# Optimization experiments

Hardware: AMD Instinct MI355X
Metric: run time of the kernel (lower is better)

## Reference

```python
import jax, jax.numpy as jnp
import numpy as np

ALPHA = 16.0
R = 8.0
SCALE = ALPHA / R  # scaling = alpha / r, same for every adapter


def setup_inputs() -> dict:
    key = jax.random.key(0)
    ks = jax.random.split(key, 5)
    B_, S, D = 4, 2048, 4096
    E, r = 8, 8
    x = jax.random.normal(ks[0], (B_, S, D), dtype=jnp.float32)
    W = jax.random.normal(ks[1], (D, D), dtype=jnp.float32) * (1.0 / np.sqrt(D))
    b = jax.random.normal(ks[2], (D,), dtype=jnp.float32) * 0.02
    A = jax.random.normal(ks[3], (E, r, D), dtype=jnp.float32) * (1.0 / np.sqrt(D))
    Bm = jax.random.normal(ks[4], (E, D, r), dtype=jnp.float32) * 0.02
    return {"x": x, "W": W, "b": b, "A": A, "B": Bm}


def reference(x, W, b, A, B):
    # base = F.linear(x, W, b)
    base = jnp.einsum('bsi,oi->bso', x, W) + b
    # lora_total = sum_e scale * (x @ A_e.T @ B_e.T); all experts stacked.
    # intermediate [B,S,E,r] is tiny (r=8)
    t = jnp.einsum('bsi,eri->bser', x, A)
    lora = jnp.einsum('bser,eor->bso', t, B) * SCALE
    return base + lora
```

## Files before the change

### kernel.cpp

```cpp
#include <hip/hip_runtime.h>
#include <hip/hip_bf16.h>

typedef unsigned short u16;
typedef __bf16 bf16x8 __attribute__((ext_vector_type(8)));
typedef float f32x4 __attribute__((ext_vector_type(4)));

constexpr int Mdim = 8192;
constexpr int Ndim = 4096;
constexpr int Kdim = 4096;
constexpr int ER   = 64;
constexpr float LSCALE = 2.0f;

__device__ __forceinline__ u16 f2bf(float f) {
    union { float f; unsigned u; } v; v.f = f;
    unsigned r = v.u + 0x7fffu + ((v.u >> 16) & 1u);
    return (u16)(r >> 16);
}

#define GLOAD_LDS16(g, l)                                             \
    __builtin_amdgcn_global_load_lds(                                 \
        (const __attribute__((address_space(1))) void*)(g),           \
        (__attribute__((address_space(3))) void*)(l), 16, 0, 0)

__global__ __launch_bounds__(256) void weff_kernel(
    const float* __restrict__ W, const float* __restrict__ A,
    const float* __restrict__ Bm, u16* __restrict__ Wb)
{
    __shared__ __align__(16) float sAc[ER][128];
    __shared__ __align__(16) float sBc[64][ER];

    const int t  = threadIdx.x;
    const int i0 = blockIdx.x * 128;
    const int o0 = blockIdx.y * 64;

#pragma unroll
    for (int p = 0; p < 8; ++p) {
        int lin = p * 1024 + t * 4;
        int er = lin >> 7, ci = lin & 127;
        *(float4*)&sAc[er][ci] = *(const float4*)(A + (size_t)er * Kdim + i0 + ci);
    }
    {
        int ol = t >> 2;
        int c  = (t & 3) * 16;
#pragma unroll
        for (int q = 0; q < 2; ++q) {
            int er = c + q * 8;
            int e  = er >> 3;
            const float* src = Bm + ((size_t)e * Ndim + (o0 + ol)) * 8;
            *(float4*)&sBc[ol][er]     = *(const float4*)(src);
            *(float4*)&sBc[ol][er + 4] = *(const float4*)(src + 4);
        }
    }
    __syncthreads();

    const int tx = t & 31;
    const int ty = t >> 5;
    float acc[8][4] = {};
#pragma unroll 4
    for (int er = 0; er < ER; ++er) {
        float4 a = *(const float4*)&sAc[er][tx * 4];
#pragma unroll
        for (int q = 0; q < 8; ++q) {
            float bv = sBc[q * 8 + ty][er];
            acc[q][0] += bv * a.x;
            acc[q][1] += bv * a.y;
            acc[q][2] += bv * a.z;
            acc[q][3] += bv * a.w;
        }
    }
#pragma unroll
    for (int q = 0; q < 8; ++q) {
        int o = o0 + q * 8 + ty;
        const float4 w = *(const float4*)(W + (size_t)o * Kdim + i0 + tx * 4);
        ushort4 st;
        st.x = f2bf(w.x + LSCALE * acc[q][0]);
        st.y = f2bf(w.y + LSCALE * acc[q][1]);
        st.z = f2bf(w.z + LSCALE * acc[q][2]);
        st.w = f2bf(w.w + LSCALE * acc[q][3]);
        *(ushort4*)(Wb + (size_t)o * Kdim + i0 + tx * 4) = st;
    }
}

__global__ __launch_bounds__(256) void cvt_x_kernel(
    const float* __restrict__ x, u16* __restrict__ xb)
{
    size_t i = (size_t)blockIdx.x * blockDim.x + threadIdx.x;
    const float4 v0 = *(const float4*)(x + i * 8);
    const float4 v1 = *(const float4*)(x + i * 8 + 4);
    uint4 o;
    o.x = (unsigned)f2bf(v0.x) | ((unsigned)f2bf(v0.y) << 16);
    o.y = (unsigned)f2bf(v0.z) | ((unsigned)f2bf(v0.w) << 16);
    o.z = (unsigned)f2bf(v1.x) | ((unsigned)f2bf(v1.y) << 16);
    o.w = (unsigned)f2bf(v1.z) | ((unsigned)f2bf(v1.w) << 16);
    *(uint4*)(xb + i * 8) = o;
}

constexpr int BM = 256, BN = 256, BK = 64;
constexpr int NT = Kdim / BK;

__global__ __launch_bounds__(512, 2) void gemm_bias_kernel(
    const u16* __restrict__ Xb, const u16* __restrict__ Wb,
    const float* __restrict__ bias, float* __restrict__ C)
{
    __shared__ __align__(16) u16 lds[65536];

    const int t    = threadIdx.x;
    const int lane = t & 63;
    const int wv   = t >> 6;
    const int wr   = wv >> 2;
    const int wc   = wv & 3;

    const int wg  = blockIdx.x;
    const int xcd = wg & 7, lid = wg >> 3;
    const int mt  = (xcd & 1) * 16 + (lid >> 2);
    const int ntl = (xcd >> 1) * 4 + (lid & 3);
    const int bm  = mt * BM;
    const int bn  = ntl * BN;

    u16* b0 = lds;
    u16* b1 = lds + 32768;

    const u16* gSrc[8]; int dOff[8];
#pragma unroll
    for (int i = 0; i < 8; ++i) {
        const int sub = i & 3;
        const int isB = i >> 2;
        const int c   = sub * 512 + t;
        const int row = c >> 3;
        const int scl = ((c ^ row) & 7) * 8;
        gSrc[i] = (isB ? Wb + (size_t)(bn + row) * Kdim
                       : Xb + (size_t)(bm + row) * Kdim) + scl;
        dOff[i] = isB * 16384 + c * 8;
    }

    const int fr  = lane & 15;
    const int cp0 = (((lane >> 4)    ) ^ (lane & 7)) * 8;
    const int cp1 = (((lane >> 4) + 4) ^ (lane & 7)) * 8;

    f32x4 acc[8][4];
#pragma unroll
    for (int i = 0; i < 8; ++i)
#pragma unroll
        for (int j = 0; j < 4; ++j)
            acc[i][j] = f32x4{0.f, 0.f, 0.f, 0.f};

    bf16x8 af[4][2];
    bf16x8 bfr[4][2];

#define DS_AF(BUF, MH)                                                        \
    _Pragma("unroll")                                                         \
    for (int mi = 0; mi < 4; ++mi) {                                          \
        const int rb = (wr * 128 + (MH) * 64 + mi * 16 + fr) * 64;            \
        af[mi][0] = *(const bf16x8*)&(BUF)[rb + cp0];                         \
        af[mi][1] = *(const bf16x8*)&(BUF)[rb + cp1];                         \
    }

#define DS_BF(BUF, NH)                                                        \
    _Pragma("unroll")                                                         \
    for (int nl = 0; nl < 2; ++nl) {                                          \
        const int ni = (NH) * 2 + nl;                                         \
        const int rb = 16384 + (wc * 64 + ni * 16 + fr) * 64;                 \
        bfr[ni][0] = *(const bf16x8*)&(BUF)[rb + cp0];                        \
        bfr[ni][1] = *(const bf16x8*)&(BUF)[rb + cp1];                        \
    }

#define MQ(MH, NH)                                                            \
    __builtin_amdgcn_s_setprio(1);                                            \
    _Pragma("unroll")                                                         \
    for (int mi = 0; mi < 4; ++mi)                                            \
        _Pragma("unroll")                                                     \
        for (int nl = 0; nl < 2; ++nl) {                                      \
            const int ni = (NH) * 2 + nl;                                     \
            acc[(MH)*4 + mi][ni] = __builtin_amdgcn_mfma_f32_16x16x32_bf16(   \
                af[mi][0], bfr[ni][0], acc[(MH)*4 + mi][ni], 0, 0, 0);        \
            acc[(MH)*4 + mi][ni] = __builtin_amdgcn_mfma_f32_16x16x32_bf16(   \
                af[mi][1], bfr[ni][1], acc[(MH)*4 + mi][ni], 0, 0, 0);        \
        }                                                                     \
    __builtin_amdgcn_s_setprio(0);

#define FENCE asm volatile("" ::: "memory")
#define BAR   __builtin_amdgcn_s_barrier(); FENCE
#define LGKM0 asm volatile("s_waitcnt lgkmcnt(0)" ::: "memory");              \
              __builtin_amdgcn_sched_barrier(0)

#define ITER(CUR, NXT, DOISS, VMS)                                            \
    {                                                                         \
        if (DOISS) {                                                          \
            _Pragma("unroll")                                                 \
            for (int i = 0; i < 8; ++i)                                       \
                GLOAD_LDS16(gSrc[i] + koff, (NXT) + dOff[i]);                 \
            koff += 64;                                                       \
        }                                                                     \
        asm volatile("s_waitcnt vmcnt(" VMS ")" ::: "memory");                \
        BAR;                                                                  \
        DS_AF(CUR, 0); DS_BF(CUR, 0);                                         \
        asm volatile("s_waitcnt lgkmcnt(8)" ::: "memory");                    \
        BAR;                                                                  \
        LGKM0; MQ(0, 0);                                                      \
        BAR;                                                                  \
        DS_BF(CUR, 1);                                                        \
        BAR;                                                                  \
        LGKM0; MQ(0, 1);                                                      \
        BAR;                                                                  \
        DS_AF(CUR, 1);                                                        \
        BAR;                                                                  \
        LGKM0; MQ(1, 1);                                                      \
        BAR;                                                                  \
        MQ(1, 0);                                                             \
    }

#pragma unroll
    for (int i = 0; i < 8; ++i) GLOAD_LDS16(gSrc[i], b0 + dOff[i]);

    int koff = 64;

#pragma unroll 1
    for (int t2 = 0; t2 < (NT - 2) / 2; ++t2) {
        ITER(b0, b1, 1, "8");
        ITER(b1, b0, 1, "8");
    }
    ITER(b0, b1, 1, "8");
    ITER(b1, b0, 0, "0");

#undef ITER
#undef MQ
#undef DS_BF
#undef DS_AF

#pragma unroll
    for (int ni = 0; ni < 4; ++ni) {
        const int col = bn + wc * 64 + ni * 16 + (lane & 15);
        const float bv = bias[col];
#pragma unroll
        for (int mi = 0; mi < 8; ++mi) {
            const int rbase = bm + wr * 128 + mi * 16 + (lane >> 4) * 4;
#pragma unroll
            for (int j = 0; j < 4; ++j)
                C[(size_t)(rbase + j) * Ndim + col] = acc[mi][ni][j] + bv;
        }
    }
}

__global__ __launch_bounds__(256) void naive_row_kernel(
    const float* __restrict__ x, const float* __restrict__ W,
    const float* __restrict__ bias, const float* __restrict__ A,
    const float* __restrict__ Bm, float* __restrict__ out)
{
    __shared__ float sx[Kdim];
    __shared__ float st[ER];
    const int m = blockIdx.x;
    const float* xr = x + (size_t)m * Kdim;
    for (int i = threadIdx.x; i < Kdim; i += 256) sx[i] = xr[i];
    __syncthreads();
    if (threadIdx.x < ER) {
        const float* ar = A + (size_t)threadIdx.x * Kdim;
        float s = 0.f;
        for (int i = 0; i < Kdim; ++i) s += sx[i] * ar[i];
        st[threadIdx.x] = s;
    }
    __syncthreads();
    for (int o = threadIdx.x; o < Ndim; o += 256) {
        const float* wr = W + (size_t)o * Kdim;
        float s = bias[o];
        for (int i = 0; i < Kdim; ++i) s += sx[i] * wr[i];
        float l = 0.f;
        for (int e = 0; e < 8; ++e) {
            const float* bp = Bm + ((size_t)e * Ndim + o) * 8;
            for (int r = 0; r < 8; ++r) l += st[e * 8 + r] * bp[r];
        }
        out[(size_t)m * Ndim + o] = s + LSCALE * l;
    }
}

extern "C" void kernel_launch(void* const* d_in, const int* in_sizes, int n_in,
                              void* d_out, int out_size, void* d_ws, size_t ws_size,
                              hipStream_t stream)
{
    const float* x  = (const float*)d_in[0];
    const float* W  = (const float*)d_in[1];
    const float* b  = (const float*)d_in[2];
    const float* A  = (const float*)d_in[3];
    const float* Bm = (const float*)d_in[4];
    float* out = (float*)d_out;

    const size_t xb_bytes = (size_t)Mdim * Kdim * 2;
    const size_t wb_bytes = (size_t)Ndim * Kdim * 2;

    if (ws_size >= xb_bytes + wb_bytes) {
        u16* Xb = (u16*)d_ws;
        u16* Wb = (u16*)((char*)d_ws + xb_bytes);
        cvt_x_kernel<<<(Mdim * (size_t)Kdim) / 8 / 256, 256, 0, stream>>>(x, Xb);
        weff_kernel<<<dim3(Kdim / 128, Ndim / 64), 256, 0, stream>>>(W, A, Bm, Wb);
        gemm_bias_kernel<<<dim3((Mdim / BM) * (Ndim / BN)), 512, 0, stream>>>(Xb, Wb, b, out);
    } else {
        naive_row_kernel<<<Mdim, 256, 0, stream>>>(x, W, b, A, Bm, out);
    }
}
```

Baseline: 312.1 us.

## Restructure GEMM main loop to defer last MFMA quadrant and cut barriers

Reorganizes the double-buffered K loop so the final MFMA quadrant of each tile is issued after the next tile's wait and barrier, overlapping it with the next global-to-LDS prefetch. The number of workgroup barriers per tile drops from seven to three and the vmcnt wait becomes a full drain at the top of each tile. This aims to reduce barrier stalls, but a vmcnt(0) wait issued before the new prefetch means the global loads are less overlapped with the wait point. That could expose memory latency and add LDS hazards.

Measured after the change: 293.1 us. -6.1%, faster.

```diff
diff --git a/kernel.cpp b/kernel.cpp
--- a/kernel.cpp
+++ b/kernel.cpp
@@ -183,30 +183,29 @@
 #define LGKM0 asm volatile("s_waitcnt lgkmcnt(0)" ::: "memory");              \
               __builtin_amdgcn_sched_barrier(0)
 
-#define ITER(CUR, NXT, DOISS, VMS)                                            \
+#define TILE(CUR, NXT, FIRST, LAST)                                           \
     {                                                                         \
-        if (DOISS) {                                                          \
+        asm volatile("s_waitcnt vmcnt(0)" ::: "memory");                      \
+        BAR;                                                                  \
+        if (!(FIRST)) { MQ(1, 0); }                                           \
+        if (!(LAST)) {                                                        \
             _Pragma("unroll")                                                 \
             for (int i = 0; i < 8; ++i)                                       \
                 GLOAD_LDS16(gSrc[i] + koff, (NXT) + dOff[i]);                 \
             koff += 64;                                                       \
         }                                                                     \
-        asm volatile("s_waitcnt vmcnt(" VMS ")" ::: "memory");                \
-        BAR;                                                                  \
-        DS_AF(CUR, 0); DS_BF(CUR, 0);                                         \
-        asm volatile("s_waitcnt lgkmcnt(8)" ::: "memory");                    \
-        BAR;                                                                  \
-        LGKM0; MQ(0, 0);                                                      \
+        DS_AF(CUR, 0);                                                        \
+        DS_BF(CUR, 0);                                                        \
+        LGKM0;                                                                \
+        MQ(0, 0);                                                             \
         BAR;                                                                  \
         DS_BF(CUR, 1);                                                        \
-        BAR;                                                                  \
-        LGKM0; MQ(0, 1);                                                      \
-        BAR;                                                                  \
+        LGKM0;                                                                \
+        MQ(0, 1);                                                             \
         DS_AF(CUR, 1);                                                        \
         BAR;                                                                  \
-        LGKM0; MQ(1, 1);                                                      \
-        BAR;                                                                  \
-        MQ(1, 0);                                                             \
+        LGKM0;                                                                \
+        MQ(1, 1);                                                             \
     }
 
 #pragma unroll
@@ -214,15 +213,16 @@
 
     int koff = 64;
 
+    TILE(b0, b1, 1, 0);
 #pragma unroll 1
     for (int t2 = 0; t2 < (NT - 2) / 2; ++t2) {
-        ITER(b0, b1, 1, "8");
-        ITER(b1, b0, 1, "8");
-    }
-    ITER(b0, b1, 1, "8");
-    ITER(b1, b0, 0, "0");
-
-#undef ITER
+        TILE(b1, b0, 0, 0);
+        TILE(b0, b1, 0, 0);
+    }
+    TILE(b1, b0, 0, 1);
+    MQ(1, 0);
+
+#undef TILE
 #undef MQ
 #undef DS_BF
 #undef DS_AF
```
